# Performance work log

Measured on AMD Instinct MI355X. Metric: run time of the kernel, lower is better.

## Reference

```python
import jax, jax.numpy as jnp
import numpy as np

DIM = 1024
N_HEADS = 16
DIM_FF = 4096
EPS = 1e-12


def layer_norm(x, gamma, beta):
    u = jnp.mean(x, axis=-1, keepdims=True)
    s = jnp.mean((x - u) ** 2, axis=-1, keepdims=True)
    return gamma * ((x - u) / jnp.sqrt(s + EPS)) + beta


def setup_inputs() -> dict:
    key = jax.random.key(0)
    ks = jax.random.split(key, 12)
    B, S, D, F = 2, 2048, DIM, DIM_FF
    init = lambda k, shape: (jax.random.normal(k, shape, dtype=jnp.float32) * 0.02)
    return {
        "x": jax.random.normal(ks[0], (B, S, D), dtype=jnp.float32),
        "mask": jnp.ones((B, S), dtype=jnp.int32),
        "wq": init(ks[1], (D, D)), "bq": jnp.zeros((D,), jnp.float32),
        "wk": init(ks[2], (D, D)), "bk": jnp.zeros((D,), jnp.float32),
        "wv": init(ks[3], (D, D)), "bv": jnp.zeros((D,), jnp.float32),
        "wo": init(ks[4], (D, D)), "bo": jnp.zeros((D,), jnp.float32),
        "g1": jnp.ones((D,), jnp.float32), "b1": jnp.zeros((D,), jnp.float32),
        "w1": init(ks[5], (D, F)), "bf1": jnp.zeros((F,), jnp.float32),
        "w2": init(ks[6], (F, D)), "bf2": jnp.zeros((D,), jnp.float32),
        "g2": jnp.ones((D,), jnp.float32), "b2": jnp.zeros((D,), jnp.float32),
    }


def reference(x, mask, wq, bq, wk, bk, wv, bv, wo, bo, g1, b1, w1, bf1, w2, bf2, g2, b2):
    B, S, D = x.shape
    H = N_HEADS
    W = D // H
    # QKV projections -> (B, H, S, W)
    def heads(y):
        return y.reshape(B, S, H, W).transpose(0, 2, 1, 3)
    q = heads(x @ wq + bq)
    k = heads(x @ wk + bk)
    v = heads(x @ wv + bv)
    # scaled dot-product attention with additive mask (exact module math)
    scores = jnp.einsum('bhsw,bhtw->bhst', q, k) / np.sqrt(W).astype(np.float32)
    m = mask.astype(jnp.float32)[:, None, None, :]  # (B,1,1,S)
    scores = scores - 10000.0 * (1.0 - m)
    attn = jax.nn.softmax(scores, axis=-1)
    h = jnp.einsum('bhst,bhtw->bhsw', attn, v).transpose(0, 2, 1, 3).reshape(B, S, D)
    # residual + LN1
    h = layer_norm(x + (h @ wo + bo), g1, b1)
    # position-wise FFN with exact-erf GELU, residual + LN2
    ff = jax.nn.gelu(h @ w1 + bf1, approximate=False) @ w2 + bf2
    return layer_norm(h + ff, g2, b2)
```

## Files before the change

kernel.cpp:

```cpp
#include <hip/hip_runtime.h>
#include <cstdint>
#include <cstddef>

using u16 = unsigned short;
using u32 = unsigned int;

typedef __bf16 bf16x8 __attribute__((ext_vector_type(8)));
typedef float f32x4 __attribute__((ext_vector_type(4)));

static constexpr int Bb = 2, S = 2048, D = 1024, H = 16, W = 64, F = 4096;
static constexpr int M = Bb * S;

__device__ __forceinline__ float bf2f(u16 u) {
  union { u32 i; float f; } c; c.i = ((u32)u) << 16; return c.f;
}
__device__ __forceinline__ u16 f2bf(float f) {
  union { float f; u32 i; } c; c.f = f;
  u32 i = c.i;
  u32 r = (i + 0x7fffu + ((i >> 16) & 1u)) >> 16;
  return (u16)r;
}
__device__ __forceinline__ u16 f2bf_cvt(float f) {
  __bf16 b = (__bf16)f;
  union { __bf16 b; u16 u; } c; c.b = b; return c.u;
}
__device__ __forceinline__ __bf16 u2b(u16 x) {
  union { u16 u; __bf16 b; } c; c.u = x; return c.b;
}
__device__ __forceinline__ void stv(float* p, size_t i, float v) { p[i] = v; }
__device__ __forceinline__ void stv(u16* p, size_t i, float v)   { p[i] = f2bf(v); }
__device__ __forceinline__ float ldv(const float* p, size_t i) { return p[i]; }
__device__ __forceinline__ float ldv(const u16* p, size_t i)   { return bf2f(p[i]); }

__device__ __forceinline__ void async_cp16(const u16* g, u16* l) {
  __builtin_amdgcn_global_load_lds(
      (const __attribute__((address_space(1))) void*)g,
      (__attribute__((address_space(3))) void*)l, 16, 0, 0);
}

__device__ __forceinline__ void swizzle8(int& bx, int& by) {
  int bid = blockIdx.y * gridDim.x + blockIdx.x;
  int gpr = gridDim.x >> 3;
  int grp = bid >> 6, rem = bid & 63;
  int gm = grp / gpr, gn = grp - gm * gpr;
  by = gm * 8 + (rem >> 3);
  bx = gn * 8 + (rem & 7);
}

__global__ __launch_bounds__(256) void conv_x_kernel(
    const float* __restrict__ src, u16* __restrict__ dst)
{
  int i = (blockIdx.x * 256 + threadIdx.x) * 4;
  float4 v = *(const float4*)(src + i);
  u16 r[4] = { f2bf(v.x), f2bf(v.y), f2bf(v.z), f2bf(v.w) };
  *(uint2*)(dst + i) = *(const uint2*)r;
}

__global__ __launch_bounds__(256) void transpose_w_kernel(
    const float* __restrict__ src, u16* __restrict__ dst, int K, int N)
{
  __shared__ __align__(16) u16 T[64][72];
  const int tid = threadIdx.x;
  const int n0 = blockIdx.x * 64, k0 = blockIdx.y * 64;
#pragma unroll
  for (int t = 0; t < 4; t++) {
    int idx = tid + t * 256;
    int r = idx >> 4, c4 = (idx & 15) * 4;
    float4 v = *(const float4*)(src + (size_t)(k0 + r) * N + n0 + c4);
    T[c4 + 0][r] = f2bf(v.x); T[c4 + 1][r] = f2bf(v.y);
    T[c4 + 2][r] = f2bf(v.z); T[c4 + 3][r] = f2bf(v.w);
  }
  __syncthreads();
#pragma unroll
  for (int t = 0; t < 2; t++) {
    int idx = tid + t * 256;
    int r = idx >> 3, c8 = (idx & 7) * 8;
    *(uint4*)(dst + (size_t)(n0 + r) * K + k0 + c8) = *(const uint4*)(&T[r][c8]);
  }
}

template<int EPI, typename TC>
__global__ __launch_bounds__(256) void gemm_bt(
    const u16* __restrict__ A, const u16* __restrict__ BT,
    const float* __restrict__ bias, TC* __restrict__ C,
    int N, int K, float scale)
{
  __shared__ __align__(16) u16 As[2][128 * 32];
  __shared__ __align__(16) u16 Bs[2][128 * 32];
  const int tid = threadIdx.x;
  const int wave = tid >> 6, lane = tid & 63;
  const int quad = lane >> 4, l16 = lane & 15;
  int bx, by; swizzle8(bx, by);
  const int m0 = by * 128, n0 = bx * 128;
  const int wm = (wave >> 1) * 64, wn = (wave & 1) * 64;
  const int srow = lane >> 2;
  const int skoff = (lane & 3) * 8;

  f32x4 acc[4][4] = {};

  for (int k0 = 0; k0 < K; k0 += 64) {
#pragma unroll
    for (int h = 0; h < 2; h++) {
#pragma unroll
      for (int t = 0; t < 2; t++) {
        int slot = wave * 2 + t;
        int row = slot * 16 + srow;
        const u16* ga = A  + (size_t)(m0 + row) * K + k0 + h * 32 + skoff;
        const u16* gb = BT + (size_t)(n0 + row) * K + k0 + h * 32 + skoff;
        async_cp16(ga, As[h] + slot * 512);
        async_cp16(gb, Bs[h] + slot * 512);
      }
    }
    __syncthreads();

#pragma unroll
    for (int h = 0; h < 2; h++) {
      bf16x8 af[4], bfv[4];
#pragma unroll
      for (int i = 0; i < 4; i++)
        af[i] = *(const bf16x8*)(As[h] + (wm + i * 16 + l16) * 32 + quad * 8);
#pragma unroll
      for (int j = 0; j < 4; j++)
        bfv[j] = *(const bf16x8*)(Bs[h] + (wn + j * 16 + l16) * 32 + quad * 8);
#pragma unroll
      for (int i = 0; i < 4; i++)
#pragma unroll
        for (int j = 0; j < 4; j++)
          acc[i][j] = __builtin_amdgcn_mfma_f32_16x16x32_bf16(af[i], bfv[j], acc[i][j], 0, 0, 0);
    }
    __syncthreads();
  }

#pragma unroll
  for (int i = 0; i < 4; i++) {
#pragma unroll
    for (int j = 0; j < 4; j++) {
#pragma unroll
      for (int r = 0; r < 4; r++) {
        int row = m0 + wm + i * 16 + quad * 4 + r;
        int col = n0 + wn + j * 16 + l16;
        float val = acc[i][j][r] + bias[col];
        if (EPI == 1) {
          val = 0.5f * val * (1.0f + erff(val * 0.70710678118654752f));
        }
        if (EPI == 2) {
          int sel = col >> 10, c = col & 1023;
          if (sel == 0) val *= scale;
          int bb = row >> 11, ss = row & 2047;
          int hh = c >> 6,  ww = c & 63;
          u16* dst = (u16*)C + (size_t)sel * M * D;
          dst[(((size_t)(bb * H + hh) * S) + ss) * W + ww] = f2bf(val);
        } else {
          stv(C, (size_t)row * N + col, val);
        }
      }
    }
  }
}

template<typename TC>
__global__ __launch_bounds__(256) void gemm_bt_n64(
    const u16* __restrict__ A, const u16* __restrict__ BT,
    const float* __restrict__ bias, TC* __restrict__ C,
    int N, int K)
{
  __shared__ __align__(16) u16 As[2][128 * 32];
  __shared__ __align__(16) u16 Bs[2][64 * 32];
  const int tid = threadIdx.x;
  const int wave = tid >> 6, lane = tid & 63;
  const int quad = lane >> 4, l16 = lane & 15;
  int bx, by; swizzle8(bx, by);
  const int m0 = by * 128, n0 = bx * 64;
  const int wm = (wave >> 1) * 64, wn = (wave & 1) * 32;
  const int srow = lane >> 2;
  const int skoff = (lane & 3) * 8;

  f32x4 acc[4][2] = {};

  for (int k0 = 0; k0 < K; k0 += 64) {
#pragma unroll
    for (int h = 0; h < 2; h++) {
#pragma unroll
      for (int t = 0; t < 2; t++) {
        int slot = wave * 2 + t;
        int row = slot * 16 + srow;
        async_cp16(A + (size_t)(m0 + row) * K + k0 + h * 32 + skoff, As[h] + slot * 512);
      }
      int row = wave * 16 + srow;
      async_cp16(BT + (size_t)(n0 + row) * K + k0 + h * 32 + skoff, Bs[h] + wave * 512);
    }
    __syncthreads();

#pragma unroll
    for (int h = 0; h < 2; h++) {
      bf16x8 af[4], bfv[2];
#pragma unroll
      for (int i = 0; i < 4; i++)
        af[i] = *(const bf16x8*)(As[h] + (wm + i * 16 + l16) * 32 + quad * 8);
#pragma unroll
      for (int j = 0; j < 2; j++)
        bfv[j] = *(const bf16x8*)(Bs[h] + (wn + j * 16 + l16) * 32 + quad * 8);
#pragma unroll
      for (int i = 0; i < 4; i++)
#pragma unroll
        for (int j = 0; j < 2; j++)
          acc[i][j] = __builtin_amdgcn_mfma_f32_16x16x32_bf16(af[i], bfv[j], acc[i][j], 0, 0, 0);
    }
    __syncthreads();
  }

#pragma unroll
  for (int i = 0; i < 4; i++) {
#pragma unroll
    for (int j = 0; j < 2; j++) {
#pragma unroll
      for (int r = 0; r < 4; r++) {
        int row = m0 + wm + i * 16 + quad * 4 + r;
        int col = n0 + wn + j * 16 + l16;
        stv(C, (size_t)row * N + col, acc[i][j][r] + bias[col]);
      }
    }
  }
}

__global__ __launch_bounds__(256) void transpose_v_kernel(
    const u16* __restrict__ v, u16* __restrict__ vt)
{
  __shared__ __align__(16) u16 T[64][72];
  const int bh = blockIdx.y, k0 = blockIdx.x * 64, tid = threadIdx.x;
#pragma unroll
  for (int it = 0; it < 2; it++) {
    int vv = tid + it * 256;
    int key = vv >> 3, w0 = (vv & 7) * 8;
    union { uint4 q; u16 e[8]; } u;
    u.q = *(const uint4*)(v + ((size_t)bh * S + k0 + key) * W + w0);
#pragma unroll
    for (int j = 0; j < 8; j++) T[w0 + j][key] = u.e[j];
  }
  __syncthreads();
#pragma unroll
  for (int it = 0; it < 2; it++) {
    int vv = tid + it * 256;
    int w = vv >> 3, koff = (vv & 7) * 8;
    *(uint4*)(vt + ((size_t)bh * W + w) * S + k0 + koff) = *(const uint4*)(&T[w][koff]);
  }
}

__global__ __launch_bounds__(256) void fattn_kernel(
    const u16* __restrict__ q, const u16* __restrict__ k,
    const u16* __restrict__ vt, const int* __restrict__ mask,
    u16* __restrict__ out)
{
  __shared__ __align__(16) u16 QP[2][64][32];
  __shared__ __align__(16) u16 Kl[2][64][32];
  __shared__ __align__(16) u16 Vl[2][64][32];
  __shared__ float msk[64];

  const int tid = threadIdx.x, wave = tid >> 6, lane = tid & 63;
  const int quad = lane >> 4, l16 = lane & 15;
  const int bh = blockIdx.y, b = bh >> 4, h = bh & 15;
  const int q0 = blockIdx.x * 64;
  const int w16 = wave * 16;
  const int sr  = tid >> 3;
  const int sg  = tid & 7;
  const int sp  = sg >> 2;
  const int sc0 = sg * 8;
  const int ssw = (((sg & 3) ^ ((sr >> 1) & 3)) << 3);
  const int rq = ((quad ^ ((l16 >> 1) & 3)) << 3);

  *(uint4*)(&QP[sp][sr     ][ssw]) = *(const uint4*)(q + ((size_t)bh * S + q0 + sr     ) * W + sc0);
  *(uint4*)(&QP[sp][sr + 32][ssw]) = *(const uint4*)(q + ((size_t)bh * S + q0 + sr + 32) * W + sc0);
  __syncthreads();
  bf16x8 aq[2];
#pragma unroll
  for (int kc = 0; kc < 2; kc++)
    aq[kc] = *(const bf16x8*)(&QP[kc][w16 + l16][rq]);

  bf16x8 ones;
  {
    u16 ov = (l16 == 0) ? (u16)0x3F80 : (u16)0;
#pragma unroll
    for (int j = 0; j < 8; j++) ones[j] = u2b(ov);
  }

  f32x4 o_acc[4] = {};
  f32x4 l_acc = {};

  uint4 kr0, kr1, vr0, vr1;
  int mv = 0;
  kr0 = *(const uint4*)(k  + ((size_t)bh * S + sr     ) * W + sc0);
  kr1 = *(const uint4*)(k  + ((size_t)bh * S + sr + 32) * W + sc0);
  vr0 = *(const uint4*)(vt + ((size_t)bh * W + sr     ) * S + sc0);
  vr1 = *(const uint4*)(vt + ((size_t)bh * W + sr + 32) * S + sc0);
  if (tid < 64) mv = mask[b * S + tid];

  for (int kt = 0; kt < S / 64; kt++) {
    __syncthreads();
    *(uint4*)(&Kl[sp][sr     ][ssw]) = kr0;
    *(uint4*)(&Kl[sp][sr + 32][ssw]) = kr1;
    *(uint4*)(&Vl[sp][sr     ][ssw]) = vr0;
    *(uint4*)(&Vl[sp][sr + 32][ssw]) = vr1;
    if (tid < 64) msk[tid] = -10000.0f * (1.0f - (float)mv);
    __syncthreads();

    if (kt + 1 < S / 64) {
      int kn = (kt + 1) * 64;
      kr0 = *(const uint4*)(k  + ((size_t)bh * S + kn + sr     ) * W + sc0);
      kr1 = *(const uint4*)(k  + ((size_t)bh * S + kn + sr + 32) * W + sc0);
      vr0 = *(const uint4*)(vt + ((size_t)bh * W + sr     ) * S + kn + sc0);
      vr1 = *(const uint4*)(vt + ((size_t)bh * W + sr + 32) * S + kn + sc0);
      if (tid < 64) mv = mask[b * S + kn + tid];
    }

    f32x4 sc[4] = {};
#pragma unroll
    for (int tn = 0; tn < 4; tn++) {
#pragma unroll
      for (int kc = 0; kc < 2; kc++) {
        bf16x8 bk = *(const bf16x8*)(&Kl[kc][tn * 16 + l16][rq]);
        sc[tn] = __builtin_amdgcn_mfma_f32_16x16x32_bf16(aq[kc], bk, sc[tn], 0, 0, 0);
      }
    }
#pragma unroll
    for (int tn = 0; tn < 4; tn++) {
      float mm = msk[tn * 16 + l16];
      int s0 = (tn & 1) * 2 + (l16 >> 3);
#pragma unroll
      for (int r = 0; r < 4; r++) {
        float pv = __expf(sc[tn][r] + mm);
        int xr = (quad * 2 + (r >> 1)) & 3;
        QP[tn >> 1][w16 + quad * 4 + r][((s0 ^ xr) << 3) | (l16 & 7)] = f2bf_cvt(pv);
      }
    }

#pragma unroll
    for (int kc = 0; kc < 2; kc++) {
      bf16x8 ap = *(const bf16x8*)(&QP[kc][w16 + l16][rq]);
#pragma unroll
      for (int tn = 0; tn < 4; tn++) {
        bf16x8 bv = *(const bf16x8*)(&Vl[kc][tn * 16 + l16][rq]);
        o_acc[tn] = __builtin_amdgcn_mfma_f32_16x16x32_bf16(ap, bv, o_acc[tn], 0, 0, 0);
      }
      l_acc = __builtin_amdgcn_mfma_f32_16x16x32_bf16(ap, ones, l_acc, 0, 0, 0);
    }
  }

#pragma unroll
  for (int r = 0; r < 4; r++) {
    float lsum = __shfl(l_acc[r], lane & 0x30);
    float inv = 1.0f / lsum;
    int sg2 = q0 + w16 + quad * 4 + r;
#pragma unroll
    for (int tn = 0; tn < 4; tn++) {
      out[((size_t)b * S + sg2) * D + h * W + tn * 16 + l16] = f2bf_cvt(o_acc[tn][r] * inv);
    }
  }
}

template<typename TA, typename TR, typename TO>
__global__ __launch_bounds__(256) void ln_res_kernel(
    const TA* __restrict__ a, const TR* __restrict__ r,
    const float* __restrict__ g, const float* __restrict__ be,
    TO* __restrict__ out)
{
  const int tid = threadIdx.x, lane = tid & 63;
  const int row = blockIdx.x * 4 + (tid >> 6);
  const TA* ap = a + (size_t)row * D;
  const TR* rp = r + (size_t)row * D;
  float hv[16];
  float s = 0.f;
#pragma unroll
  for (int c = 0; c < 16; c++) {
    int d = c * 64 + lane;
    hv[c] = ldv(ap, d) + ldv(rp, d);
    s += hv[c];
  }
#pragma unroll
  for (int d = 1; d < 64; d <<= 1) s += __shfl_xor(s, d);
  float mean = s * (1.0f / D);
  float v = 0.f;
#pragma unroll
  for (int c = 0; c < 16; c++) { float t = hv[c] - mean; v += t * t; }
#pragma unroll
  for (int d = 1; d < 64; d <<= 1) v += __shfl_xor(v, d);
  float inv = rsqrtf(v * (1.0f / D) + 1e-12f);
#pragma unroll
  for (int c = 0; c < 16; c++) {
    int d = c * 64 + lane;
    stv(out, (size_t)row * D + d, g[d] * ((hv[c] - mean) * inv) + be[d]);
  }
}

extern "C" void kernel_launch(void* const* d_in, const int* in_sizes, int n_in,
                              void* d_out, int out_size, void* d_ws, size_t ws_size,
                              hipStream_t stream)
{
  const float* x  = (const float*)d_in[0];
  const int* mask = (const int*)d_in[1];
  const float* wq = (const float*)d_in[2];  const float* bq  = (const float*)d_in[3];
  const float* wk = (const float*)d_in[4];  const float* bk  = (const float*)d_in[5];
  const float* wv = (const float*)d_in[6];  const float* bv  = (const float*)d_in[7];
  const float* wo = (const float*)d_in[8];  const float* bo  = (const float*)d_in[9];
  const float* g1 = (const float*)d_in[10]; const float* b1  = (const float*)d_in[11];
  const float* w1 = (const float*)d_in[12]; const float* bf1 = (const float*)d_in[13];
  const float* w2 = (const float*)d_in[14]; const float* bf2 = (const float*)d_in[15];
  const float* g2 = (const float*)d_in[16]; const float* b2  = (const float*)d_in[17];

  char* ws = (char*)d_ws;
  const size_t MB = 1024 * 1024;
  u16* wqkvT = (u16*)(ws + 0 * MB);
  u16* woT   = (u16*)(ws + 6 * MB);
  u16* w1T   = (u16*)(ws + 0 * MB);
  u16* w2T   = (u16*)(ws + 0 * MB);
  u16* xb    = (u16*)(ws + 8 * MB);
  u16* vt    = (u16*)(ws + 8 * MB);
  u16* q     = (u16*)(ws + 16 * MB);
  u16* proj  = (u16*)(ws + 16 * MB);
  u16* kb    = (u16*)(ws + 24 * MB);
  u16* vb    = (u16*)(ws + 32 * MB);
  u16* attn  = (u16*)(ws + 32 * MB);
  u16* ff1   = (u16*)(ws + 8 * MB);
  float* bqkv = (float*)(ws + 40 * MB);
  u16* h1    = (u16*)(ws + 40 * MB);
  float* out = (float*)d_out;

  dim3 blk(256);

  conv_x_kernel<<<dim3(M * D / 1024), blk, 0, stream>>>(x, xb);
  transpose_w_kernel<<<dim3(16, 16), blk, 0, stream>>>(wq, wqkvT,            D, D);
  transpose_w_kernel<<<dim3(16, 16), blk, 0, stream>>>(wk, wqkvT + 1024*1024, D, D);
  transpose_w_kernel<<<dim3(16, 16), blk, 0, stream>>>(wv, wqkvT + 2048*1024, D, D);
  transpose_w_kernel<<<dim3(16, 16), blk, 0, stream>>>(wo, woT,              D, D);
  hipMemcpyAsync(bqkv,        bq, D * sizeof(float), hipMemcpyDeviceToDevice, stream);
  hipMemcpyAsync(bqkv + 1024, bk, D * sizeof(float), hipMemcpyDeviceToDevice, stream);
  hipMemcpyAsync(bqkv + 2048, bv, D * sizeof(float), hipMemcpyDeviceToDevice, stream);

  gemm_bt<2, u16><<<dim3(3072 / 128, M / 128), blk, 0, stream>>>(
      xb, wqkvT, bqkv, q, 3072, D, 0.125f);

  transpose_v_kernel<<<dim3(S / 64, Bb * H), blk, 0, stream>>>(vb, vt);
  fattn_kernel<<<dim3(S / 64, Bb * H), blk, 0, stream>>>(q, kb, vt, mask, attn);

  gemm_bt_n64<u16><<<dim3(D / 64, M / 128), blk, 0, stream>>>(
      attn, woT, bo, proj, D, D);
  ln_res_kernel<float, u16, u16><<<dim3(M / 4), blk, 0, stream>>>(x, proj, g1, b1, h1);

  transpose_w_kernel<<<dim3(F / 64, D / 64), blk, 0, stream>>>(w1, w1T, D, F);
  gemm_bt<1, u16><<<dim3(F / 128, M / 128), blk, 0, stream>>>(
      h1, w1T, bf1, ff1, F, D, 1.0f);

  transpose_w_kernel<<<dim3(D / 64, F / 64), blk, 0, stream>>>(w2, w2T, F, D);
  gemm_bt_n64<float><<<dim3(D / 64, M / 128), blk, 0, stream>>>(
      ff1, w2T, bf2, out, D, F);
  ln_res_kernel<u16, float, float><<<dim3(M / 4), blk, 0, stream>>>(h1, out, g2, b2, out);
}
```

Before: 430.1 us.

## Split attention over two key halves and merge partial results in a combine kernel

The flash-attention kernel now gets a third grid dimension that splits the key range in half. Each half writes its unnormalized bf16 output and its row sums to workspace buffers. A new combine kernel adds the two halves and normalizes. This doubles the number of blocks to improve GPU occupancy and load balance, at the cost of an extra memory pass and one more bf16 rounding of the partial outputs.

```diff
diff --git a/kernel.cpp b/kernel.cpp
--- a/kernel.cpp
+++ b/kernel.cpp
@@ -249,7 +249,7 @@
 __global__ __launch_bounds__(256) void fattn_kernel(
     const u16* __restrict__ q, const u16* __restrict__ k,
     const u16* __restrict__ vt, const int* __restrict__ mask,
-    u16* __restrict__ out)
+    u16* __restrict__ o_parts, float* __restrict__ l_parts)
 {
   __shared__ __align__(16) u16 QP[2][64][32];
   __shared__ __align__(16) u16 Kl[2][64][32];
@@ -260,6 +260,8 @@
   const int quad = lane >> 4, l16 = lane & 15;
   const int bh = blockIdx.y, b = bh >> 4, h = bh & 15;
   const int q0 = blockIdx.x * 64;
+  const int half = blockIdx.z;
+  const int kbase = half * (S / 2);
   const int w16 = wave * 16;
   const int sr  = tid >> 3;
   const int sg  = tid & 7;
@@ -288,13 +290,14 @@
 
   uint4 kr0, kr1, vr0, vr1;
   int mv = 0;
-  kr0 = *(const uint4*)(k  + ((size_t)bh * S + sr     ) * W + sc0);
-  kr1 = *(const uint4*)(k  + ((size_t)bh * S + sr + 32) * W + sc0);
-  vr0 = *(const uint4*)(vt + ((size_t)bh * W + sr     ) * S + sc0);
-  vr1 = *(const uint4*)(vt + ((size_t)bh * W + sr + 32) * S + sc0);
-  if (tid < 64) mv = mask[b * S + tid];
-
-  for (int kt = 0; kt < S / 64; kt++) {
+  kr0 = *(const uint4*)(k  + ((size_t)bh * S + kbase + sr     ) * W + sc0);
+  kr1 = *(const uint4*)(k  + ((size_t)bh * S + kbase + sr + 32) * W + sc0);
+  vr0 = *(const uint4*)(vt + ((size_t)bh * W + sr     ) * S + kbase + sc0);
+  vr1 = *(const uint4*)(vt + ((size_t)bh * W + sr + 32) * S + kbase + sc0);
+  if (tid < 64) mv = mask[b * S + kbase + tid];
+
+  constexpr int NT = S / 128;
+  for (int kt = 0; kt < NT; kt++) {
     __syncthreads();
     *(uint4*)(&Kl[sp][sr     ][ssw]) = kr0;
     *(uint4*)(&Kl[sp][sr + 32][ssw]) = kr1;
@@ -303,8 +306,8 @@
     if (tid < 64) msk[tid] = -10000.0f * (1.0f - (float)mv);
     __syncthreads();
 
-    if (kt + 1 < S / 64) {
-      int kn = (kt + 1) * 64;
+    if (kt + 1 < NT) {
+      int kn = kbase + (kt + 1) * 64;
       kr0 = *(const uint4*)(k  + ((size_t)bh * S + kn + sr     ) * W + sc0);
       kr1 = *(const uint4*)(k  + ((size_t)bh * S + kn + sr + 32) * W + sc0);
       vr0 = *(const uint4*)(vt + ((size_t)bh * W + sr     ) * S + kn + sc0);
@@ -345,16 +348,36 @@
     }
   }
 
+  u16* ob = o_parts + (size_t)half * M * D;
+  float* lb = l_parts + (size_t)half * M * H;
 #pragma unroll
   for (int r = 0; r < 4; r++) {
     float lsum = __shfl(l_acc[r], lane & 0x30);
-    float inv = 1.0f / lsum;
     int sg2 = q0 + w16 + quad * 4 + r;
+    if (l16 == 0) lb[((size_t)b * S + sg2) * H + h] = lsum;
 #pragma unroll
     for (int tn = 0; tn < 4; tn++) {
-      out[((size_t)b * S + sg2) * D + h * W + tn * 16 + l16] = f2bf_cvt(o_acc[tn][r] * inv);
-    }
-  }
+      ob[((size_t)b * S + sg2) * D + h * W + tn * 16 + l16] = f2bf_cvt(o_acc[tn][r]);
+    }
+  }
+}
+
+__global__ __launch_bounds__(256) void combine_attn(
+    const u16* __restrict__ o_parts, const float* __restrict__ l_parts,
+    u16* __restrict__ attn)
+{
+  size_t idx = ((size_t)blockIdx.x * 256 + threadIdx.x) * 8;
+  int row = (int)(idx >> 10);
+  int h = ((int)idx >> 6) & 15;
+  float l = l_parts[(size_t)row * H + h] + l_parts[(size_t)M * H + (size_t)row * H + h];
+  float inv = 1.0f / l;
+  union { uint4 v; u16 e[8]; } a, bq, o;
+  a.v  = *(const uint4*)(o_parts + idx);
+  bq.v = *(const uint4*)(o_parts + (size_t)M * D + idx);
+#pragma unroll
+  for (int j = 0; j < 8; j++)
+    o.e[j] = f2bf((bf2f(a.e[j]) + bf2f(bq.e[j])) * inv);
+  *(uint4*)(attn + idx) = o.v;
 }
 
 template<typename TA, typename TR, typename TO>
@@ -418,6 +441,8 @@
   u16* proj  = (u16*)(ws + 16 * MB);
   u16* kb    = (u16*)(ws + 24 * MB);
   u16* vb    = (u16*)(ws + 32 * MB);
+  u16* oparts = (u16*)(ws + 32 * MB);
+  float* lparts = (float*)(ws + 0 * MB);
   u16* attn  = (u16*)(ws + 32 * MB);
   u16* ff1   = (u16*)(ws + 8 * MB);
   float* bqkv = (float*)(ws + 40 * MB);
@@ -439,7 +464,9 @@
       xb, wqkvT, bqkv, q, 3072, D, 0.125f);
 
   transpose_v_kernel<<<dim3(S / 64, Bb * H), blk, 0, stream>>>(vb, vt);
-  fattn_kernel<<<dim3(S / 64, Bb * H), blk, 0, stream>>>(q, kb, vt, mask, attn);
+  fattn_kernel<<<dim3(S / 64, Bb * H, 2), blk, 0, stream>>>(
+      q, kb, vt, mask, oparts, lparts);
+  combine_attn<<<dim3(M * D / 2048), blk, 0, stream>>>(oparts, lparts, attn);
 
   gemm_bt_n64<u16><<<dim3(D / 64, M / 128), blk, 0, stream>>>(
       attn, woT, bo, proj, D, D);
```

Result: no change. 425.7 us (-1.0%).
